# Performance work log

Measured on AMD Instinct MI355X. Metric: run time of the kernel, lower is better.

## Reference

```python
import jax, jax.numpy as jnp
import numpy as np


def _pairwise_sqdist(x, y):
    # x: [B,N,D], y: [B,M,D] -> P: [B,N,M] squared euclidean distances
    xx = jnp.sum(x * x, axis=-1)            # [B,N]
    yy = jnp.sum(y * y, axis=-1)            # [B,M]
    zz = jnp.einsum('bnd,bmd->bnm', x, y)   # [B,N,M]
    return xx[:, :, None] + yy[:, None, :] - 2.0 * zz


def setup_inputs() -> dict:
    key = jax.random.key(0)
    k1, k2 = jax.random.split(key)
    B, N, M, D = 8, 4096, 4096, 256
    gts = jax.random.normal(k1, (B, N, D), dtype=jnp.float32)
    preds = jax.random.normal(k2, (B, M, D), dtype=jnp.float32)
    return {"gts": gts, "preds": preds}


def reference(gts, preds):
    P = _pairwise_sqdist(gts, preds)        # [B,N,M]
    loss_1 = jnp.sum(jnp.min(P, axis=1))    # min over gts dim (axis=1)
    loss_2 = jnp.sum(jnp.min(P, axis=2))    # min over preds dim (axis=2)
    return loss_1 + loss_2
```

## Files before the change

### kernel.cpp

```cpp
#include <hip/hip_runtime.h>

typedef int   i32x8 __attribute__((ext_vector_type(8)));
typedef float f32x4 __attribute__((ext_vector_type(4)));

#define B_   8
#define N_   4096
#define D_   256


__device__ __forceinline__ void gl_lds16(const void* g, void* l) {
  __builtin_amdgcn_global_load_lds(
      (const __attribute__((address_space(1))) unsigned int*)g,
      (__attribute__((address_space(3))) unsigned int*)l, 16, 0, 0);
}

__device__ __forceinline__ float sq8(unsigned w) {
  float f0 = __builtin_amdgcn_cvt_f32_fp8(w, 0);
  float f1 = __builtin_amdgcn_cvt_f32_fp8(w, 1);
  float f2 = __builtin_amdgcn_cvt_f32_fp8(w, 2);
  float f3 = __builtin_amdgcn_cvt_f32_fp8(w, 3);
  return f0 * f0 + f1 * f1 + f2 * f2 + f3 * f3;
}

__global__ __launch_bounds__(256) void prep_kernel(
    const float* __restrict__ x, const float* __restrict__ y,
    unsigned char* __restrict__ Xf, unsigned char* __restrict__ Yf,
    float* __restrict__ xx, float* __restrict__ yy,
    unsigned* __restrict__ rowmin, unsigned* __restrict__ colmin,
    float* __restrict__ out)
{
  __shared__ unsigned char T[4][16 * 272];
  if (blockIdx.x == 0 && threadIdx.x == 0) out[0] = 0.f;

  const int wv = threadIdx.x >> 6, lane = threadIdx.x & 63;
  const int wid = (blockIdx.x << 2) + wv;

  const float* src; unsigned char* dst; float* nrm; unsigned* mn; int g;
  if (wid < 2048) { g = wid;        src = x; dst = Xf; nrm = xx; mn = rowmin; }
  else            { g = wid - 2048; src = y; dst = Yf; nrm = yy; mn = colmin; }

  unsigned char* tw = T[wv];
  const float* rp = src + (size_t)g * 16 * D_;
#pragma unroll
  for (int r = 0; r < 16; ++r) {
    float4 v = *(const float4*)(rp + r * D_ + lane * 4);
    unsigned u = __builtin_amdgcn_cvt_pk_fp8_f32(v.x, v.y, 0, 0);
    u = __builtin_amdgcn_cvt_pk_fp8_f32(v.z, v.w, u, 1);
    *(unsigned*)(tw + r * 272 + lane * 4) = u;
  }
  asm volatile("s_waitcnt lgkmcnt(0)" ::: "memory");
  __builtin_amdgcn_wave_barrier();

  float s = 0.f;
  const int row = lane & 15, ko = (lane >> 4) * 32;
#pragma unroll
  for (int kt = 0; kt < 2; ++kt)
#pragma unroll
    for (int h = 0; h < 2; ++h) {
      uint4 c = *(const uint4*)(tw + row * 272 + kt * 128 + ko + h * 16);
      s += sq8(c.x) + sq8(c.y) + sq8(c.z) + sq8(c.w);
      *(uint4*)(dst + ((((size_t)g * 2 + kt) * 2 + h) << 10) + lane * 16) = c;
    }
  s += __shfl_xor(s, 16, 64);
  s += __shfl_xor(s, 32, 64);
  if      (lane < 16) nrm[g * 16 + lane] = s;
  else if (lane < 32) mn[g * 16 + lane - 16] = 0x7f800000u;
}

__global__ __launch_bounds__(256, 2) void chamfer_gemm(
    const unsigned char* __restrict__ Xf, const unsigned char* __restrict__ Yf,
    const float* __restrict__ xx, const float* __restrict__ yy,
    unsigned* __restrict__ rowmin, unsigned* __restrict__ colmin)
{
  __shared__ __align__(16) unsigned char S[4][8192];
  __shared__ unsigned cmin_s[512];

  const int bid = blockIdx.x;
  const int b   = bid & 7;
  const int rt  = (bid >> 3) & 15;
  const int cq  = bid >> 7;
  const int n0  = rt * 256;
  const int m0  = cq * 512;

  const int t = threadIdx.x, lane = t & 63, wave = t >> 6;
  const int quad = lane >> 4, lcol = lane & 15;

  cmin_s[t]       = 0x7f800000u;
  cmin_s[t + 256] = 0x7f800000u;

  i32x8 af[4][2];
#pragma unroll
  for (int i = 0; i < 4; ++i) {
    const size_t g = (size_t)(b * 256 + rt * 16 + wave * 4 + i);
#pragma unroll
    for (int kt = 0; kt < 2; ++kt) {
      const uint4* p = (const uint4*)(Xf + ((g * 2 + kt) << 11));
      uint4* h = (uint4*)&af[i][kt];
      h[0] = p[lane];
      h[1] = p[64 + lane];
    }
  }

  float xv[4][4], rmin[4][4];
  const float* xxp = xx + b * N_ + n0 + wave * 64;
#pragma unroll
  for (int i = 0; i < 4; ++i)
#pragma unroll
    for (int r = 0; r < 4; ++r) {
      xv[i][r] = xxp[i * 16 + quad * 4 + r];
      rmin[i][r] = 1e30f;
    }

  const unsigned char* Ybase = Yf + ((size_t)(b * 256 + cq * 32) << 12);
  const float* yyp = yy + b * N_ + m0;

#define STAGE_B(ct_, buf_)                                                    \
  {                                                                           \
    const unsigned char* Ysrc = Ybase + ((size_t)(ct_) << 13);     \
    _Pragma("unroll")                                                         \
    for (int h2 = 0; h2 < 2; ++h2) {                                          \
      int s  = t + h2 * 256;                                                  \
      int cd = s >> 6, ln = s & 63;                                           \
      int kt = cd >> 2, hh = (cd >> 1) & 1, jj = cd & 1;                      \
      gl_lds16(Ysrc + jj * 4096 + kt * 2048 + hh * 1024 + ln * 16,            \
               (buf_) + s * 16);                                              \
    }                                                                         \
  }

  auto do_ct = [&](int ct, const unsigned char* curb) {
    float yv0 = yyp[ct * 32 + lcol];
    float yv1 = yyp[ct * 32 + 16 + lcol];

    i32x8 bq[2][2];
#pragma unroll
    for (int j = 0; j < 2; ++j)
#pragma unroll
      for (int kt = 0; kt < 2; ++kt) {
        uint4* h = (uint4*)&bq[j][kt];
        h[0] = *(const uint4*)(curb + (kt * 4 + 0 + j) * 1024 + lane * 16);
        h[1] = *(const uint4*)(curb + (kt * 4 + 2 + j) * 1024 + lane * 16);
      }

    f32x4 acc[4][2] = {};
    __builtin_amdgcn_s_setprio(1);
#pragma unroll
    for (int kt = 0; kt < 2; ++kt)
#pragma unroll
      for (int i = 0; i < 4; ++i)
#pragma unroll
        for (int j = 0; j < 2; ++j)
          acc[i][j] = __builtin_amdgcn_mfma_scale_f32_16x16x128_f8f6f4(
              af[i][kt], bq[j][kt], acc[i][j],
              0, 0,
              0, 127,
              0, 127);
    __builtin_amdgcn_s_setprio(0);

#pragma unroll
    for (int j = 0; j < 2; ++j) {
      float yv = j ? yv1 : yv0;
      float tc[16];
#pragma unroll
      for (int i = 0; i < 4; ++i)
#pragma unroll
        for (int r = 0; r < 4; ++r) {
          float a = acc[i][j][r];
          rmin[i][r] = fminf(rmin[i][r], __builtin_fmaf(-2.0f, a, yv));
          tc[i * 4 + r] = __builtin_fmaf(-2.0f, a, xv[i][r]);
        }
      float m0_ = fminf(fminf(tc[0], tc[1]), fminf(tc[2], tc[3]));
      float m1_ = fminf(fminf(tc[4], tc[5]), fminf(tc[6], tc[7]));
      float m2_ = fminf(fminf(tc[8], tc[9]), fminf(tc[10], tc[11]));
      float m3_ = fminf(fminf(tc[12], tc[13]), fminf(tc[14], tc[15]));
      float cm  = fminf(fminf(m0_, m1_), fminf(m2_, m3_));
      atomicMin(&cmin_s[ct * 32 + j * 16 + lcol], __float_as_uint(cm + yv));
    }
  };

  STAGE_B(0, S[0]);
  STAGE_B(1, S[1]);

  for (int g = 0; g < 8; ++g) {
    __syncthreads();
    const int cur = (g & 1) * 2;
    if (g + 1 < 8) {
      const int nxt = ((g + 1) & 1) * 2;
      STAGE_B(2 * g + 2, S[nxt]);
      STAGE_B(2 * g + 3, S[nxt + 1]);
    }
    do_ct(2 * g,     S[cur]);
    do_ct(2 * g + 1, S[cur + 1]);
  }

#pragma unroll
  for (int i = 0; i < 4; ++i)
#pragma unroll
    for (int r = 0; r < 4; ++r) {
      float v = xv[i][r] + rmin[i][r];
#pragma unroll
      for (int m = 1; m < 16; m <<= 1) v = fminf(v, __shfl_xor(v, m, 64));
      if (lcol == 0)
        atomicMin(rowmin + b * N_ + n0 + wave * 64 + i * 16 + quad * 4 + r,
                  __float_as_uint(v));
    }

  __syncthreads();
#pragma unroll
  for (int i = 0; i < 2; ++i) {
    int idx = t + i * 256;
    atomicMin(colmin + b * N_ + m0 + idx, cmin_s[idx]);
  }
#undef STAGE_B
}

__global__ __launch_bounds__(256) void reduce_kernel(
    const unsigned* __restrict__ mins,
    float* __restrict__ out)
{
  int idx = blockIdx.x * 256 + threadIdx.x;
  uint4 u = ((const uint4*)mins)[idx];
  float s = __uint_as_float(u.x) + __uint_as_float(u.y)
          + __uint_as_float(u.z) + __uint_as_float(u.w);
#pragma unroll
  for (int m = 1; m < 64; m <<= 1) s += __shfl_xor(s, m, 64);
  if ((threadIdx.x & 63) == 0) atomicAdd(out, s);
}

extern "C" void kernel_launch(void* const* d_in, const int* in_sizes, int n_in,
                              void* d_out, int out_size, void* d_ws, size_t ws_size,
                              hipStream_t stream) {
  const float* gts   = (const float*)d_in[0];
  const float* preds = (const float*)d_in[1];

  char* ws = (char*)d_ws;
  const size_t XB_BYTES = (size_t)B_ * N_ * D_;
  unsigned char* Xf     = (unsigned char*)ws;
  unsigned char* Yf     = (unsigned char*)(ws + XB_BYTES);
  float*    xx     = (float*)(ws + 2 * XB_BYTES);
  float*    yy     = (float*)(ws + 2 * XB_BYTES + (size_t)B_ * N_ * 4);
  unsigned* rowmin = (unsigned*)(ws + 2 * XB_BYTES + (size_t)B_ * N_ * 8);
  unsigned* colmin = (unsigned*)(ws + 2 * XB_BYTES + (size_t)B_ * N_ * 12);

  prep_kernel<<<1024, 256, 0, stream>>>(gts, preds, Xf, Yf, xx, yy, rowmin, colmin,
                                        (float*)d_out);

  chamfer_gemm<<<1024, 256, 0, stream>>>(Xf, Yf, xx, yy, rowmin, colmin);

  reduce_kernel<<<64, 256, 0, stream>>>(rowmin, (float*)d_out);
}
```

Before: 134.9 us.

## Software-pipeline chamfer GEMM with triple-buffered LDS and interleaved epilogue

Restructures the main loop into a ping-pong schedule. The epilogue (min reductions) of the previous column tile is interleaved with the MFMA phase of the next one, using two accumulator sets and explicit barriers with sched_barrier fences. Y tiles are triple-buffered in LDS and waited on with explicit vmcnt counts. The yy norms are preloaded into LDS. The goal is to overlap VALU epilogue work and global-to-LDS loads with matrix-core work, at the cost of more LDS and registers, many extra barriers, and fragile hand-set waitcnt accounting.

Measured after the change: 407.9 us. 202% more time.

```diff
diff --git a/kernel.cpp b/kernel.cpp
--- a/kernel.cpp
+++ b/kernel.cpp
@@ -67,13 +67,17 @@
   else if (lane < 32) mn[g * 16 + lane - 16] = 0x7f800000u;
 }
 
+#define SB() __builtin_amdgcn_sched_barrier(0)
+#define PBAR() do { SB(); __builtin_amdgcn_s_barrier(); SB(); } while (0)
+
 __global__ __launch_bounds__(256, 2) void chamfer_gemm(
     const unsigned char* __restrict__ Xf, const unsigned char* __restrict__ Yf,
     const float* __restrict__ xx, const float* __restrict__ yy,
     unsigned* __restrict__ rowmin, unsigned* __restrict__ colmin)
 {
-  __shared__ __align__(16) unsigned char S[4][8192];
+  __shared__ __align__(16) unsigned char S[6][8192];
   __shared__ unsigned cmin_s[512];
+  __shared__ float    yys[512];
 
   const int bid = blockIdx.x;
   const int b   = bid & 7;
@@ -87,6 +91,10 @@
 
   cmin_s[t]       = 0x7f800000u;
   cmin_s[t + 256] = 0x7f800000u;
+  const float* yyp = yy + b * N_ + m0;
+  if (t < 128)
+    gl_lds16((const unsigned char*)yyp + t * 16, (unsigned char*)yys + t * 16);
+  __syncthreads();
 
   i32x8 af[4][2];
 #pragma unroll
@@ -112,7 +120,6 @@
     }
 
   const unsigned char* Ybase = Yf + ((size_t)(b * 256 + cq * 32) << 12);
-  const float* yyp = yy + b * N_ + m0;
 
 #define STAGE_B(ct_, buf_)                                                    \
   {                                                                           \
@@ -127,70 +134,105 @@
     }                                                                         \
   }
 
-  auto do_ct = [&](int ct, const unsigned char* curb) {
-    float yv0 = yyp[ct * 32 + lcol];
-    float yv1 = yyp[ct * 32 + 16 + lcol];
-
-    i32x8 bq[2][2];
-#pragma unroll
-    for (int j = 0; j < 2; ++j)
-#pragma unroll
-      for (int kt = 0; kt < 2; ++kt) {
-        uint4* h = (uint4*)&bq[j][kt];
-        h[0] = *(const uint4*)(curb + (kt * 4 + 0 + j) * 1024 + lane * 16);
-        h[1] = *(const uint4*)(curb + (kt * 4 + 2 + j) * 1024 + lane * 16);
+  auto RD = [&](i32x8 (&bq)[2], const unsigned char* buf, int kt) {
+#pragma unroll
+    for (int j = 0; j < 2; ++j) {
+      uint4* h = (uint4*)&bq[j];
+      h[0] = *(const uint4*)(buf + (kt * 4 + 0 + j) * 1024 + lane * 16);
+      h[1] = *(const uint4*)(buf + (kt * 4 + 2 + j) * 1024 + lane * 16);
+    }
+  };
+
+  auto MM = [&](f32x4 (&acc)[4][2], i32x8 (&bq)[2], int kt) {
+    __builtin_amdgcn_s_setprio(1);
+#pragma unroll
+    for (int i = 0; i < 4; ++i)
+#pragma unroll
+      for (int j = 0; j < 2; ++j)
+        acc[i][j] = __builtin_amdgcn_mfma_scale_f32_16x16x128_f8f6f4(
+            af[i][kt], bq[j], acc[i][j],
+            0, 0,
+            0, 127,
+            0, 127);
+    __builtin_amdgcn_s_setprio(0);
+  };
+
+  auto ZRO = [&](f32x4 (&acc)[4][2]) {
+#pragma unroll
+    for (int i = 0; i < 4; ++i)
+#pragma unroll
+      for (int j = 0; j < 2; ++j) acc[i][j] = f32x4{0.f, 0.f, 0.f, 0.f};
+  };
+
+  auto EPI = [&](f32x4 (&acc)[4][2], int ct, int j) {
+    float yv = yys[ct * 32 + j * 16 + lcol];
+    float tc[16];
+#pragma unroll
+    for (int i = 0; i < 4; ++i)
+#pragma unroll
+      for (int r = 0; r < 4; ++r) {
+        float a = acc[i][j][r];
+        rmin[i][r] = fminf(rmin[i][r], __builtin_fmaf(-2.0f, a, yv));
+        tc[i * 4 + r] = __builtin_fmaf(-2.0f, a, xv[i][r]);
       }
-
-    f32x4 acc[4][2] = {};
-    __builtin_amdgcn_s_setprio(1);
-#pragma unroll
-    for (int kt = 0; kt < 2; ++kt)
-#pragma unroll
-      for (int i = 0; i < 4; ++i)
-#pragma unroll
-        for (int j = 0; j < 2; ++j)
-          acc[i][j] = __builtin_amdgcn_mfma_scale_f32_16x16x128_f8f6f4(
-              af[i][kt], bq[j][kt], acc[i][j],
-              0, 0,
-              0, 127,
-              0, 127);
-    __builtin_amdgcn_s_setprio(0);
-
-#pragma unroll
-    for (int j = 0; j < 2; ++j) {
-      float yv = j ? yv1 : yv0;
-      float tc[16];
-#pragma unroll
-      for (int i = 0; i < 4; ++i)
-#pragma unroll
-        for (int r = 0; r < 4; ++r) {
-          float a = acc[i][j][r];
-          rmin[i][r] = fminf(rmin[i][r], __builtin_fmaf(-2.0f, a, yv));
-          tc[i * 4 + r] = __builtin_fmaf(-2.0f, a, xv[i][r]);
-        }
-      float m0_ = fminf(fminf(tc[0], tc[1]), fminf(tc[2], tc[3]));
-      float m1_ = fminf(fminf(tc[4], tc[5]), fminf(tc[6], tc[7]));
-      float m2_ = fminf(fminf(tc[8], tc[9]), fminf(tc[10], tc[11]));
-      float m3_ = fminf(fminf(tc[12], tc[13]), fminf(tc[14], tc[15]));
-      float cm  = fminf(fminf(m0_, m1_), fminf(m2_, m3_));
-      atomicMin(&cmin_s[ct * 32 + j * 16 + lcol], __float_as_uint(cm + yv));
-    }
+    float m0_ = fminf(fminf(tc[0], tc[1]), fminf(tc[2], tc[3]));
+    float m1_ = fminf(fminf(tc[4], tc[5]), fminf(tc[6], tc[7]));
+    float m2_ = fminf(fminf(tc[8], tc[9]), fminf(tc[10], tc[11]));
+    float m3_ = fminf(fminf(tc[12], tc[13]), fminf(tc[14], tc[15]));
+    float cm  = fminf(fminf(m0_, m1_), fminf(m2_, m3_));
+    atomicMin(&cmin_s[ct * 32 + j * 16 + lcol], __float_as_uint(cm + yv));
   };
 
   STAGE_B(0, S[0]);
   STAGE_B(1, S[1]);
-
+  STAGE_B(2, S[2]);
+  STAGE_B(3, S[3]);
+  __syncthreads();
+
+  i32x8 bq0[2], bq1[2];
+  f32x4 accA[4][2], accB[4][2];
+
+#pragma unroll
   for (int g = 0; g < 8; ++g) {
-    __syncthreads();
-    const int cur = (g & 1) * 2;
-    if (g + 1 < 8) {
-      const int nxt = ((g + 1) & 1) * 2;
-      STAGE_B(2 * g + 2, S[nxt]);
-      STAGE_B(2 * g + 3, S[nxt + 1]);
-    }
-    do_ct(2 * g,     S[cur]);
-    do_ct(2 * g + 1, S[cur + 1]);
-  }
+    const int ctA = 2 * g, ctB = 2 * g + 1;
+    const unsigned char* bufA = S[2 * (g % 3)];
+    const unsigned char* bufB = S[2 * (g % 3) + 1];
+    unsigned char* stA = S[2 * ((g + 2) % 3)];
+    unsigned char* stB = S[2 * ((g + 2) % 3) + 1];
+
+    if (g > 0) EPI(accB, ctA - 1, 0);
+    ZRO(accA);
+    RD(bq0, bufA, 0);
+    if (g <= 5) STAGE_B(2 * (g + 2), stA);
+    PBAR();
+    MM(accA, bq0, 0);
+    PBAR();
+
+    if (g > 0) EPI(accB, ctA - 1, 1);
+    RD(bq1, bufA, 1);
+    if (g <= 5) STAGE_B(2 * (g + 2) + 1, stB);
+    PBAR();
+    MM(accA, bq1, 1);
+    PBAR();
+
+    EPI(accA, ctA, 0);
+    ZRO(accB);
+    RD(bq0, bufB, 0);
+    PBAR();
+    MM(accB, bq0, 0);
+    PBAR();
+
+    EPI(accA, ctA, 1);
+    RD(bq1, bufB, 1);
+    PBAR();
+    MM(accB, bq1, 1);
+    SB();
+    if (g <= 5)      asm volatile("s_waitcnt vmcnt(4)" ::: "memory");
+    else if (g == 6) asm volatile("s_waitcnt vmcnt(0)" ::: "memory");
+    PBAR();
+  }
+  EPI(accB, 15, 0);
+  EPI(accB, 15, 1);
 
 #pragma unroll
   for (int i = 0; i < 4; ++i)
```
